# Kernel optimization log

Hardware: AMD Instinct MI355X
Metric: run time of the kernel (lower is better)

## Reference

```python
import jax, jax.numpy as jnp
import numpy as np

S_LOCAL = 3
N_HEADS = 8
EPS = 1e-6


def setup_inputs() -> dict:
    key = jax.random.key(0)
    ks = jax.random.split(key, 9)
    B, D, T, H, W = 2, 512, 96, 16, 16
    std = 0.02
    return {
        "x": jax.random.normal(ks[0], (B, D, T, H, W), dtype=jnp.float32),
        "ln_gamma": jnp.ones((D,), dtype=jnp.float32),
        "ln_beta": jnp.zeros((D,), dtype=jnp.float32),
        "Wq": jax.random.normal(ks[1], (D, D), dtype=jnp.float32) * std,
        "Wk": jax.random.normal(ks[2], (D, D), dtype=jnp.float32) * std,
        "Wv": jax.random.normal(ks[3], (D, D), dtype=jnp.float32) * std,
        "Wkl": jax.random.normal(ks[4], (D, D), dtype=jnp.float32) * std,
        "Wvl": jax.random.normal(ks[5], (D, D), dtype=jnp.float32) * std,
        "Wo": jax.random.normal(ks[6], (D, D), dtype=jnp.float32) * std,
        "q_bias": jax.random.normal(ks[7], (1, N_HEADS, 1, D // N_HEADS), dtype=jnp.float32) * std,
    }


def _unfold_windows(x, s):
    # x: [..., T] -> [..., T, s] sliding windows with zero padding s//2 each side
    p = s // 2
    xp = jnp.pad(x, [(0, 0)] * (x.ndim - 1) + [(p, p)])
    T = x.shape[-1]
    idx = jnp.arange(T)[:, None] + jnp.arange(s)[None, :]  # [T, s]
    return xp[..., idx]


def reference(x, ln_gamma, ln_beta, Wq, Wk, Wv, Wkl, Wvl, Wo, q_bias):
    B, D, T, H, W = x.shape
    nh, dh, s = N_HEADS, D // N_HEADS, S_LOCAL
    factor = dh ** (-0.5)
    N = B * H * W

    # [B,D,T,H,W] -> [N, T, D]
    xt = jnp.transpose(x, (0, 3, 4, 2, 1)).reshape(N, T, D)

    # LayerNorm over D
    mu = xt.mean(-1, keepdims=True)
    var = xt.var(-1, keepdims=True)
    xn = (xt - mu) / jnp.sqrt(var + EPS) * ln_gamma + ln_beta

    # projections -> [N, nh, T, dh]
    def heads(y):
        return jnp.transpose(y.reshape(N, T, nh, dh), (0, 2, 1, 3))

    q = heads(xn @ Wq.T) + q_bias
    k = heads(xn @ Wk.T)
    v = heads(xn @ Wv.T)

    # global attention scores [N, nh, T, T]
    attn_global = jnp.einsum('bhnd,bhgd->bhng', q, k) * factor

    # local k/v: [N, T, D] -> [N, D, T] -> windows [N, D, T, s]
    kl = jnp.transpose(xn @ Wkl.T, (0, 2, 1))
    vl = jnp.transpose(xn @ Wvl.T, (0, 2, 1))
    k_w = jnp.transpose(_unfold_windows(kl, s).reshape(N, nh, dh, T, s), (0, 1, 3, 2, 4))  # [N,nh,T,dh,s]
    v_w = jnp.transpose(_unfold_windows(vl, s).reshape(N, nh, dh, T, s), (0, 1, 3, 2, 4))

    # local mask: True where window element came from zero padding -> [T, s]
    mask_local = _unfold_windows(jnp.ones((T,), dtype=jnp.float32), s) == 0

    attn_local = jnp.einsum('bhnd,bhndl->bhnl', q, k_w)
    attn_local = jnp.where(mask_local, -jnp.inf, attn_local) * factor

    # joint softmax over [T global + s local]
    attn_map = jax.nn.softmax(jnp.concatenate([attn_global, attn_local], axis=-1), axis=-1)
    ag, al = attn_map[..., :T], attn_map[..., T:]

    x_global = jnp.einsum('bhng,bhgd->bhnd', ag, v)
    x_local = jnp.einsum('bhnl,bhndl->bhnd', al, v_w)

    out = (jnp.transpose(x_global + x_local, (0, 2, 1, 3)).reshape(N, T, D)) @ Wo.T
    return jnp.transpose(out.reshape(B, H, W, T, D), (0, 4, 3, 1, 2))
```

## Files before the change

### kernel.cpp

```cpp
#include <hip/hip_runtime.h>
#include <hip/hip_fp16.h>
#include <cstdint>
#include <cstddef>

typedef _Float16 f16;
typedef _Float16 half8 __attribute__((ext_vector_type(8)));
typedef _Float16 half4v __attribute__((ext_vector_type(4)));
typedef float floatx4 __attribute__((ext_vector_type(4)));

#define MTOT 49152

__device__ __forceinline__ void gload_lds16(const f16* g, f16* l) {
  __builtin_amdgcn_global_load_lds((const __attribute__((address_space(1))) void*)g,
                                   (__attribute__((address_space(3))) void*)l, 16, 0, 0);
}

__device__ __forceinline__ half8 load_h8u(const f16* p) {
  half8 v;
  __builtin_memcpy(&v, p, 16);
  return v;
}

__global__ __launch_bounds__(256) void wconv_kernel(
    const float* __restrict__ Wq, const float* __restrict__ Wk,
    const float* __restrict__ Wv, const float* __restrict__ Wkl,
    const float* __restrict__ Wvl, const float* __restrict__ Wo,
    f16* __restrict__ WQKV, f16* __restrict__ WO) {
  int idx = blockIdx.x * 256 + threadIdx.x;
  if (idx < 2560 * 512) {
    int row = idx >> 9;
    int col = idx & 511;
    int seg = row >> 9;
    int r = row & 511;
    const float* src;
    switch (seg) {
      case 0: src = Wq; break;
      case 1: src = Wk; break;
      case 2: src = Wkl; break;
      case 3: src = Wvl; break;
      default: src = Wv; break;
    }
    WQKV[idx] = (f16)src[r * 512 + col];
  }
  if (idx < 512 * 512) WO[idx] = (f16)Wo[idx];
}

__global__ __launch_bounds__(256) void ln_kernel(
    const float* __restrict__ x, const float* __restrict__ gamma,
    const float* __restrict__ beta, f16* __restrict__ XN) {
  const int hwg = blockIdx.x & 3;
  const int t   = (blockIdx.x >> 2) % 96;
  const int b   = blockIdx.x / (4 * 96);
  const int lhw = threadIdx.x & 63;
  const int dg  = threadIdx.x >> 6;
  const int hw  = hwg * 64 + lhw;
  const float* xp = x + (size_t)b * 512 * 24576 + (size_t)t * 256 + hw;

  float s = 0.f, s2 = 0.f;
  for (int d = dg * 128; d < dg * 128 + 128; ++d) {
    float v = xp[(size_t)d * 24576];
    s += v;
    s2 += v * v;
  }
  __shared__ float S1[4][64], S2[4][64];
  S1[dg][lhw] = s;
  S2[dg][lhw] = s2;
  __syncthreads();
  s  = S1[0][lhw] + S1[1][lhw] + S1[2][lhw] + S1[3][lhw];
  s2 = S2[0][lhw] + S2[1][lhw] + S2[2][lhw] + S2[3][lhw];
  const float mean = s * (1.f / 512.f);
  float var = s2 * (1.f / 512.f) - mean * mean;
  var = fmaxf(var, 0.f);
  const float rstd = rsqrtf(var + 1e-6f);
  const int n = b * 256 + hw;
  f16* outp = XN + ((size_t)n * 96 + t) * 512;
  for (int d0 = dg * 128; d0 < dg * 128 + 128; d0 += 8) {
    half8 buf;
#pragma unroll
    for (int j = 0; j < 8; ++j) {
      float v = xp[(size_t)(d0 + j) * 24576];
      buf[j] = (f16)((v - mean) * rstd * gamma[d0 + j] + beta[d0 + j]);
    }
    *(half8*)(outp + d0) = buf;
  }
}

template <int EPI>
__global__ __launch_bounds__(256) void gemm_kernel(
    const f16* __restrict__ A, const f16* __restrict__ B,
    f16* __restrict__ Cqkv, const float* __restrict__ qbias,
    float* __restrict__ Out) {
  __shared__ f16 As[2][128 * 32];
  __shared__ f16 Bs[2][128 * 32];

  const int lin = blockIdx.x;
  const int cpx = (int)gridDim.x >> 3;
  const int o = (lin & 7) * cpx + (lin >> 3);
  int mt, nt;
  if (EPI == 0) {
    mt = o / 20;
    nt = o % 20;
  } else {
    nt = o >> 2;
    mt = o & 3;
  }
  const int m0 = mt * 128;
  const int n0 = nt * 128;
  const int tid = threadIdx.x;
  const int lane = tid & 63;
  const int wid = tid >> 6;
  const int wm = wid >> 1, wn = wid & 1;
  const int l15 = lane & 15, l4 = lane >> 4;

  floatx4 acc[4][4] = {};

  const int srow = tid >> 2;
  const int skp = (((tid & 3) ^ ((tid >> 3) & 3))) * 8;
  const f16* ap = A + (size_t)(m0 + srow) * 512 + skp;
  const f16* bp = B + (size_t)(n0 + srow) * 512 + skp;

  auto stage = [&](int buf, int k0) {
    f16* asl = As[buf] + tid * 8;
    f16* bsl = Bs[buf] + tid * 8;
    gload_lds16(ap + k0, asl);
    gload_lds16(ap + (size_t)64 * 512 + k0, asl + 2048);
    gload_lds16(bp + k0, bsl);
    gload_lds16(bp + (size_t)64 * 512 + k0, bsl + 2048);
  };

  const int rc = (l4 ^ ((l15 >> 1) & 3)) * 8;

  stage(0, 0);
  __syncthreads();
  int cur = 0;
  for (int k0 = 0; k0 < 512; k0 += 32) {
    if (k0 + 32 < 512) stage(cur ^ 1, k0 + 32);
    half8 af[4], bf[4];
#pragma unroll
    for (int mf = 0; mf < 4; ++mf)
      af[mf] = *(const half8*)(As[cur] + (wm * 64 + mf * 16 + l15) * 32 + rc);
#pragma unroll
    for (int nf = 0; nf < 4; ++nf)
      bf[nf] = *(const half8*)(Bs[cur] + (wn * 64 + nf * 16 + l15) * 32 + rc);
#pragma unroll
    for (int mf = 0; mf < 4; ++mf)
#pragma unroll
      for (int nf = 0; nf < 4; ++nf)
        acc[mf][nf] = __builtin_amdgcn_mfma_f32_16x16x32_f16(af[mf], bf[nf], acc[mf][nf], 0, 0, 0);
    __syncthreads();
    cur ^= 1;
  }

  const int mbase = m0 + wm * 64;
  const int nbase = n0 + wn * 64;
  if constexpr (EPI == 0) {
    __shared__ __align__(16) f16 esc[4][16][72];
    float bias[4], scl[4];
#pragma unroll
    for (int nf = 0; nf < 4; ++nf) {
      const int n = nbase + nf * 16 + l15;
      const bool isq = (n < 512);
      bias[nf] = isq ? qbias[n] : 0.0f;
      scl[nf] = isq ? 0.125f : 1.0f;
    }
    const int rrow = lane >> 2;
    const int rcg = lane & 3;
#pragma unroll
    for (int mf = 0; mf < 4; ++mf) {
#pragma unroll
      for (int nf = 0; nf < 4; ++nf)
#pragma unroll
        for (int j = 0; j < 4; ++j)
          esc[wid][l4 * 4 + j][nf * 16 + l15] = (f16)((acc[mf][nf][j] + bias[nf]) * scl[nf]);
      asm volatile("s_waitcnt lgkmcnt(0)" ::: "memory");
      half8 v0 = *(const half8*)(&esc[wid][rrow][rcg * 16]);
      half8 v1 = *(const half8*)(&esc[wid][rrow][rcg * 16 + 8]);
      asm volatile("" ::: "memory");
      f16* dst = Cqkv + (size_t)(mbase + mf * 16 + rrow) * 2560 + nbase + rcg * 16;
      *(half8*)dst = v0;
      *(half8*)(dst + 8) = v1;
    }
  } else {
#pragma unroll
    for (int nf = 0; nf < 4; ++nf) {
      const int m2 = nbase + nf * 16 + l15;
      const int bb = m2 / 24576;
      const int rem = m2 - bb * 24576;
      const int t = rem >> 8;
      const int hw = rem & 255;
      float* op = Out + ((size_t)bb * 512 * 96 + t) * 256 + hw;
#pragma unroll
      for (int mf = 0; mf < 4; ++mf) {
#pragma unroll
        for (int j = 0; j < 4; ++j) {
          const int d = mbase + mf * 16 + l4 * 4 + j;
          __builtin_nontemporal_store(acc[mf][nf][j], op + (size_t)d * 24576);
        }
      }
    }
  }
}

__global__ __launch_bounds__(192) void attn_kernel(
    const f16* __restrict__ QKV, f16* __restrict__ AO, int n0chunk) {
  const int nn = blockIdx.x >> 3;
  const int h = blockIdx.x & 7;
  const int tid = threadIdx.x;
  const int wid = tid >> 6;
  const int lane = tid & 63;
  const int l15 = lane & 15, l4 = lane >> 4;
  const int nglob = n0chunk + nn;
  const int bb = nglob >> 8, hw = nglob & 255;

  __shared__ __align__(16) f16 VTl[64][112];
  __shared__ __align__(16) f16 VLTl[64][112];
  __shared__ __align__(16) float locS[3][16][4];
  __shared__ __align__(16) f16 pS[3][16][104];
  __shared__ __align__(16) f16 pS2[3][16][40];

  const f16* base = QKV + (size_t)nn * 96 * 2560;

#pragma unroll
  for (int it = 0; it < 4; ++it) {
    const int r = (tid >> 3) + it * 24;
    const int c0 = (tid & 7) * 8;
    half8 v  = *(const half8*)(base + (size_t)r * 2560 + 2048 + h * 64 + c0);
    half8 vl = *(const half8*)(base + (size_t)r * 2560 + 1536 + h * 64 + c0);
#pragma unroll
    for (int j = 0; j < 8; ++j) {
      VTl[c0 + j][r]  = v[j];
      VLTl[c0 + j][r] = vl[j];
    }
  }
  if (tid < 128) {
    half8 z = {};
    *(half8*)(&VLTl[tid >> 1][96 + (tid & 1) * 8]) = z;
  }

  half8 kb[6][2];
#pragma unroll
  for (int nf = 0; nf < 6; ++nf)
#pragma unroll
    for (int kg = 0; kg < 2; ++kg)
      kb[nf][kg] = *(const half8*)(base + (size_t)(nf * 16 + l15) * 2560 + 512 + h * 64 + kg * 32 + l4 * 8);

  __syncthreads();

  for (int mb = wid * 2; mb < wid * 2 + 2; ++mb) {
    const int t0 = mb * 16;
    const int tb = (t0 >= 2) ? (t0 - 2) : 0;
    const int d0 = t0 - 1 - tb;

    half8 aq[2], kl1[2], kl2[2];
    {
      int r1 = t0 - 1 + l15; if (r1 < 0) r1 = 0;
      int r2 = t0 + 1 + l15; if (r2 > 95) r2 = 95;
#pragma unroll
      for (int kg = 0; kg < 2; ++kg) {
        aq[kg]  = *(const half8*)(base + (size_t)(t0 + l15) * 2560 + h * 64 + kg * 32 + l4 * 8);
        kl1[kg] = *(const half8*)(base + (size_t)r1 * 2560 + 1024 + h * 64 + kg * 32 + l4 * 8);
        kl2[kg] = *(const half8*)(base + (size_t)r2 * 2560 + 1024 + h * 64 + kg * 32 + l4 * 8);
      }
    }

    floatx4 s[6] = {};
    floatx4 sl1 = {}, sl2 = {};
#pragma unroll
    for (int nf = 0; nf < 6; ++nf)
#pragma unroll
      for (int kg = 0; kg < 2; ++kg)
        s[nf] = __builtin_amdgcn_mfma_f32_16x16x32_f16(aq[kg], kb[nf][kg], s[nf], 0, 0, 0);
#pragma unroll
    for (int kg = 0; kg < 2; ++kg) {
      sl1 = __builtin_amdgcn_mfma_f32_16x16x32_f16(aq[kg], kl1[kg], sl1, 0, 0, 0);
      sl2 = __builtin_amdgcn_mfma_f32_16x16x32_f16(aq[kg], kl2[kg], sl2, 0, 0, 0);
    }

    half8 vb[4][3], vlb[4];
#pragma unroll
    for (int nf = 0; nf < 4; ++nf) {
#pragma unroll
      for (int kg = 0; kg < 3; ++kg)
        vb[nf][kg] = *(const half8*)(&VTl[nf * 16 + l15][kg * 32 + l4 * 8]);
      vlb[nf] = load_h8u(&VLTl[nf * 16 + l15][tb + l4 * 8]);
    }

    {
      half8 z = {};
      f16* pz = &pS2[wid][0][0];
      *(half8*)(pz + lane * 8) = z;
      if (lane < 16) *(half8*)(pz + 512 + lane * 8) = z;
    }
#pragma unroll
    for (int j = 0; j < 4; ++j) {
      const int r = l4 * 4 + j;
      const int s1i = l15 - r;
      if (s1i >= 0 && s1i < 3) locS[wid][r][s1i] = sl1[j];
      const int s2i = l15 + 2 - r;
      if (l15 >= 14 && s2i >= 0 && s2i < 3) locS[wid][r][s2i] = sl2[j];
    }
    __syncthreads();

#pragma unroll
    for (int j = 0; j < 4; ++j) {
      const int row = l4 * 4 + j;
      float sv[6];
#pragma unroll
      for (int nf = 0; nf < 6; ++nf) sv[nf] = s[nf][j];
      float mx = sv[0];
#pragma unroll
      for (int nf = 1; nf < 6; ++nf) mx = fmaxf(mx, sv[nf]);
      for (int off = 1; off < 16; off <<= 1) mx = fmaxf(mx, __shfl_xor(mx, off, 64));
      const float l0 = (t0 + row >= 1)  ? locS[wid][row][0] : -__builtin_inff();
      const float l1 = locS[wid][row][1];
      const float l2 = (t0 + row <= 94) ? locS[wid][row][2] : -__builtin_inff();
      mx = fmaxf(mx, fmaxf(l0, fmaxf(l1, l2)));
      float e[6], sum = 0.f;
#pragma unroll
      for (int nf = 0; nf < 6; ++nf) {
        e[nf] = expf(sv[nf] - mx);
        sum += e[nf];
      }
      for (int off = 1; off < 16; off <<= 1) sum += __shfl_xor(sum, off, 64);
      const float e0 = expf(l0 - mx), e1 = expf(l1 - mx), e2 = expf(l2 - mx);
      sum += e0 + e1 + e2;
      const float rd = 1.0f / sum;
#pragma unroll
      for (int nf = 0; nf < 6; ++nf) pS[wid][row][nf * 16 + l15] = (f16)(e[nf] * rd);
      if (l15 < 3) {
        const int w = row + l15 + d0;
        const float ev = (l15 == 0) ? e0 : ((l15 == 1) ? e1 : e2);
        if (w >= 0) pS2[wid][row][w] = (f16)(ev * rd);
      }
    }
    __syncthreads();

    floatx4 o[4] = {};
    half8 pfr[3];
#pragma unroll
    for (int kg = 0; kg < 3; ++kg)
      pfr[kg] = *(const half8*)(&pS[wid][l15][kg * 32 + l4 * 8]);
    half8 pf2 = *(const half8*)(&pS2[wid][l15][l4 * 8]);
#pragma unroll
    for (int nf = 0; nf < 4; ++nf) {
#pragma unroll
      for (int kg = 0; kg < 3; ++kg)
        o[nf] = __builtin_amdgcn_mfma_f32_16x16x32_f16(pfr[kg], vb[nf][kg], o[nf], 0, 0, 0);
      o[nf] = __builtin_amdgcn_mfma_f32_16x16x32_f16(pf2, vlb[nf], o[nf], 0, 0, 0);
    }

#pragma unroll
    for (int nf = 0; nf < 4; ++nf) {
      const int col = h * 64 + nf * 16 + l15;
#pragma unroll
      for (int j = 0; j < 4; ++j) {
        const int t = t0 + l4 * 4 + j;
        AO[((size_t)(bb * 96 + t) * 256 + hw) * 512 + col] = (f16)o[nf][j];
      }
    }
  }
}

extern "C" void kernel_launch(void* const* d_in, const int* in_sizes, int n_in,
                              void* d_out, int out_size, void* d_ws, size_t ws_size,
                              hipStream_t stream) {
  (void)in_sizes; (void)n_in; (void)out_size;
  const float* x     = (const float*)d_in[0];
  const float* gamma = (const float*)d_in[1];
  const float* beta  = (const float*)d_in[2];
  const float* Wq    = (const float*)d_in[3];
  const float* Wk    = (const float*)d_in[4];
  const float* Wv    = (const float*)d_in[5];
  const float* Wkl   = (const float*)d_in[6];
  const float* Wvl   = (const float*)d_in[7];
  const float* Wo    = (const float*)d_in[8];
  const float* qb    = (const float*)d_in[9];
  float* out = (float*)d_out;

  char* ws = (char*)d_ws;
  size_t off = 0;
  auto alloc = [&](size_t bytes) -> void* {
    void* p = ws + off;
    off += (bytes + 255) & ~(size_t)255;
    return p;
  };
  f16* XN   = (f16*)alloc((size_t)MTOT * 512 * 2);
  f16* AO   = (f16*)alloc((size_t)MTOT * 512 * 2);
  f16* WQKV = (f16*)alloc((size_t)2560 * 512 * 2);
  f16* WOh  = (f16*)alloc((size_t)512 * 512 * 2);
  int cn = 512;
  while (cn > 4 && off + (size_t)cn * 96 * 2560 * 2 + 256 > ws_size)
    cn >>= 1;
  f16* QKVc = (f16*)alloc((size_t)cn * 96 * 2560 * 2);

  wconv_kernel<<<5120, 256, 0, stream>>>(Wq, Wk, Wv, Wkl, Wvl, Wo, WQKV, WOh);
  ln_kernel<<<768, 256, 0, stream>>>(x, gamma, beta, XN);

  const int nch = 512 / cn;
  for (int c = 0; c < nch; ++c) {
    const int ng1 = (cn * 96 / 128) * 20;
    gemm_kernel<0><<<ng1, 256, 0, stream>>>(XN + (size_t)c * cn * 96 * 512, WQKV,
                                            QKVc, qb, nullptr);
    attn_kernel<<<cn * 8, 192, 0, stream>>>(QKVc, AO, c * cn);
  }
  gemm_kernel<1><<<1536, 256, 0, stream>>>(WOh, AO, nullptr, nullptr, out);
}
```

Measured before the change: 439.2 us.

## Replace QKV projection GEMM with 256x256-tile, 8-wave, ping-pong pipelined kernel

Splits the templated GEMM into a dedicated QKV-projection kernel and an output-projection kernel. The QKV kernel uses 256x256 tiles with K-step 64, 512 threads, direct global-to-LDS loads staged in quarter-tiles between MFMA phases, and s_setprio to interleave memory and compute. Larger tiles raise arithmetic intensity and cut redundant A/B fetches. The cost is much higher LDS and register pressure and tighter chunk-size constraints, with the minimum chunk raised to 32.

Result: faster. 423.7 us (-3.5%).

```diff
diff --git a/kernel.cpp b/kernel.cpp
--- a/kernel.cpp
+++ b/kernel.cpp
@@ -85,10 +85,173 @@
   }
 }
 
-template <int EPI>
-__global__ __launch_bounds__(256) void gemm_kernel(
+__global__ __launch_bounds__(512, 2) void gemmA_kernel(
     const f16* __restrict__ A, const f16* __restrict__ B,
-    f16* __restrict__ Cqkv, const float* __restrict__ qbias,
+    f16* __restrict__ Cqkv, const float* __restrict__ qbias) {
+  __shared__ f16 LA[2][256 * 64];
+  __shared__ f16 LB[2][256 * 64];
+  __shared__ __align__(16) f16 esc[8][16][72];
+
+  const int lin = blockIdx.x;
+  const int cpx = (int)gridDim.x >> 3;
+  const int swz = (lin & 7) * cpx + (lin >> 3);
+  const int o = ((gridDim.x & 7) == 0) ? swz : lin;
+  const int mt = o / 10;
+  const int nt = o % 10;
+  const int m0 = mt * 256;
+  const int n0 = nt * 256;
+
+  const int tid = threadIdx.x;
+  const int wid = tid >> 6;
+  const int lane = tid & 63;
+  const int wm = wid >> 2;
+  const int wn = wid & 3;
+  const int l15 = lane & 15, l4 = lane >> 4;
+
+  const int srow = tid >> 3;
+  const int scol = ((tid & 7) ^ (srow & 7)) * 8;
+  const f16* Abase = A + (size_t)(m0 + srow) * 512 + scol;
+  const f16* Bbase = B + (size_t)(n0 + srow) * 512 + scol;
+
+  const int cks0 = ((l4) ^ (l15 & 7)) * 8;
+  const int cks1 = ((4 + l4) ^ (l15 & 7)) * 8;
+  const int arow = wm * 128 + l15;
+  const int brow = wn * 64 + l15;
+
+  floatx4 acc[8][4] = {};
+  half8 a_f[4][2];
+  half8 b_f[4][2];
+
+  auto stageH = [&](int slot, int kt, int mat, int h) {
+    const f16* g = (mat ? Bbase : Abase) + kt * 64 + (size_t)(h * 128) * 512;
+    f16* l = (mat ? LB[slot] : LA[slot]) + h * 8192 + tid * 8;
+    gload_lds16(g, l);
+    gload_lds16(g + (size_t)64 * 512, l + 4096);
+  };
+
+  stageH(0, 0, 0, 0); stageH(0, 0, 0, 1);
+  stageH(0, 0, 1, 0); stageH(0, 0, 1, 1);
+  stageH(1, 1, 0, 0);
+  asm volatile("s_waitcnt vmcnt(2)" ::: "memory");
+  __builtin_amdgcn_s_barrier();
+
+#pragma unroll
+  for (int kt = 0; kt < 8; ++kt) {
+    const f16* As = LA[kt & 1];
+    const f16* Bs = LB[kt & 1];
+    const int nsl = (kt + 1) & 1;
+
+#pragma unroll
+    for (int mf2 = 0; mf2 < 4; ++mf2) {
+      a_f[mf2][0] = *(const half8*)(As + (arow + mf2 * 16) * 64 + cks0);
+      a_f[mf2][1] = *(const half8*)(As + (arow + mf2 * 16) * 64 + cks1);
+    }
+#pragma unroll
+    for (int nf = 0; nf < 2; ++nf) {
+      b_f[nf][0] = *(const half8*)(Bs + (brow + nf * 16) * 64 + cks0);
+      b_f[nf][1] = *(const half8*)(Bs + (brow + nf * 16) * 64 + cks1);
+    }
+    if (kt + 1 < 8) stageH(nsl, kt + 1, 0, 1);
+    __builtin_amdgcn_s_barrier();
+    __builtin_amdgcn_s_setprio(1);
+#pragma unroll
+    for (int mf2 = 0; mf2 < 4; ++mf2)
+#pragma unroll
+      for (int nf2 = 0; nf2 < 2; ++nf2)
+#pragma unroll
+        for (int ks = 0; ks < 2; ++ks)
+          acc[mf2][nf2] = __builtin_amdgcn_mfma_f32_16x16x32_f16(
+              a_f[mf2][ks], b_f[nf2][ks], acc[mf2][nf2], 0, 0, 0);
+    __builtin_amdgcn_s_setprio(0);
+    __builtin_amdgcn_s_barrier();
+
+#pragma unroll
+    for (int nf = 2; nf < 4; ++nf) {
+      b_f[nf][0] = *(const half8*)(Bs + (brow + nf * 16) * 64 + cks0);
+      b_f[nf][1] = *(const half8*)(Bs + (brow + nf * 16) * 64 + cks1);
+    }
+    if (kt + 1 < 8) stageH(nsl, kt + 1, 1, 0);
+    __builtin_amdgcn_s_barrier();
+    __builtin_amdgcn_s_setprio(1);
+#pragma unroll
+    for (int mf2 = 0; mf2 < 4; ++mf2)
+#pragma unroll
+      for (int nf2 = 0; nf2 < 2; ++nf2)
+#pragma unroll
+        for (int ks = 0; ks < 2; ++ks)
+          acc[mf2][2 + nf2] = __builtin_amdgcn_mfma_f32_16x16x32_f16(
+              a_f[mf2][ks], b_f[2 + nf2][ks], acc[mf2][2 + nf2], 0, 0, 0);
+    __builtin_amdgcn_s_setprio(0);
+    __builtin_amdgcn_s_barrier();
+
+#pragma unroll
+    for (int mf2 = 0; mf2 < 4; ++mf2) {
+      a_f[mf2][0] = *(const half8*)(As + (arow + 64 + mf2 * 16) * 64 + cks0);
+      a_f[mf2][1] = *(const half8*)(As + (arow + 64 + mf2 * 16) * 64 + cks1);
+    }
+    if (kt + 1 < 8) stageH(nsl, kt + 1, 1, 1);
+    __builtin_amdgcn_s_barrier();
+    __builtin_amdgcn_s_setprio(1);
+#pragma unroll
+    for (int mf2 = 0; mf2 < 4; ++mf2)
+#pragma unroll
+      for (int nf2 = 0; nf2 < 2; ++nf2)
+#pragma unroll
+        for (int ks = 0; ks < 2; ++ks)
+          acc[4 + mf2][nf2] = __builtin_amdgcn_mfma_f32_16x16x32_f16(
+              a_f[mf2][ks], b_f[nf2][ks], acc[4 + mf2][nf2], 0, 0, 0);
+    __builtin_amdgcn_s_setprio(0);
+    __builtin_amdgcn_s_barrier();
+
+    if (kt + 2 < 8) stageH(kt & 1, kt + 2, 0, 0);
+    __builtin_amdgcn_s_barrier();
+    __builtin_amdgcn_s_setprio(1);
+#pragma unroll
+    for (int mf2 = 0; mf2 < 4; ++mf2)
+#pragma unroll
+      for (int nf2 = 0; nf2 < 2; ++nf2)
+#pragma unroll
+        for (int ks = 0; ks < 2; ++ks)
+          acc[4 + mf2][2 + nf2] = __builtin_amdgcn_mfma_f32_16x16x32_f16(
+              a_f[mf2][ks], b_f[2 + nf2][ks], acc[4 + mf2][2 + nf2], 0, 0, 0);
+    __builtin_amdgcn_s_setprio(0);
+    if (kt < 6) {
+      asm volatile("s_waitcnt vmcnt(2)" ::: "memory");
+    } else if (kt == 6) {
+      asm volatile("s_waitcnt vmcnt(0)" ::: "memory");
+    }
+    __builtin_amdgcn_s_barrier();
+  }
+
+  float bias[4], scl[4];
+#pragma unroll
+  for (int nf = 0; nf < 4; ++nf) {
+    const int n = n0 + wn * 64 + nf * 16 + l15;
+    const bool isq = (n < 512);
+    bias[nf] = isq ? qbias[n] : 0.0f;
+    scl[nf]  = isq ? 0.125f : 1.0f;
+  }
+  const int rrow = lane >> 2;
+  const int rcg  = lane & 3;
+#pragma unroll
+  for (int mf = 0; mf < 8; ++mf) {
+#pragma unroll
+    for (int nf = 0; nf < 4; ++nf)
+#pragma unroll
+      for (int j = 0; j < 4; ++j)
+        esc[wid][l4 * 4 + j][nf * 16 + l15] = (f16)((acc[mf][nf][j] + bias[nf]) * scl[nf]);
+    asm volatile("s_waitcnt lgkmcnt(0)" ::: "memory");
+    half8 v0 = *(const half8*)(&esc[wid][rrow][rcg * 16]);
+    half8 v1 = *(const half8*)(&esc[wid][rrow][rcg * 16 + 8]);
+    asm volatile("" ::: "memory");
+    f16* dst = Cqkv + (size_t)(m0 + wm * 128 + mf * 16 + rrow) * 2560 + n0 + wn * 64 + rcg * 16;
+    *(half8*)dst = v0;
+    *(half8*)(dst + 8) = v1;
+  }
+}
+
+__global__ __launch_bounds__(256) void gemmO_kernel(
+    const f16* __restrict__ A, const f16* __restrict__ B,
     float* __restrict__ Out) {
   __shared__ f16 As[2][128 * 32];
   __shared__ f16 Bs[2][128 * 32];
@@ -96,14 +259,8 @@
   const int lin = blockIdx.x;
   const int cpx = (int)gridDim.x >> 3;
   const int o = (lin & 7) * cpx + (lin >> 3);
-  int mt, nt;
-  if (EPI == 0) {
-    mt = o / 20;
-    nt = o % 20;
-  } else {
-    nt = o >> 2;
-    mt = o & 3;
-  }
+  const int nt = o >> 2;
+  const int mt = o & 3;
   const int m0 = mt * 128;
   const int n0 = nt * 128;
   const int tid = threadIdx.x;
@@ -153,49 +310,20 @@
 
   const int mbase = m0 + wm * 64;
   const int nbase = n0 + wn * 64;
-  if constexpr (EPI == 0) {
-    __shared__ __align__(16) f16 esc[4][16][72];
-    float bias[4], scl[4];
-#pragma unroll
-    for (int nf = 0; nf < 4; ++nf) {
-      const int n = nbase + nf * 16 + l15;
-      const bool isq = (n < 512);
-      bias[nf] = isq ? qbias[n] : 0.0f;
-      scl[nf] = isq ? 0.125f : 1.0f;
-    }
-    const int rrow = lane >> 2;
-    const int rcg = lane & 3;
+#pragma unroll
+  for (int nf = 0; nf < 4; ++nf) {
+    const int m2 = nbase + nf * 16 + l15;
+    const int bb = m2 / 24576;
+    const int rem = m2 - bb * 24576;
+    const int t = rem >> 8;
+    const int hw = rem & 255;
+    float* op = Out + ((size_t)bb * 512 * 96 + t) * 256 + hw;
 #pragma unroll
     for (int mf = 0; mf < 4; ++mf) {
 #pragma unroll
-      for (int nf = 0; nf < 4; ++nf)
-#pragma unroll
-        for (int j = 0; j < 4; ++j)
-          esc[wid][l4 * 4 + j][nf * 16 + l15] = (f16)((acc[mf][nf][j] + bias[nf]) * scl[nf]);
-      asm volatile("s_waitcnt lgkmcnt(0)" ::: "memory");
-      half8 v0 = *(const half8*)(&esc[wid][rrow][rcg * 16]);
-      half8 v1 = *(const half8*)(&esc[wid][rrow][rcg * 16 + 8]);
-      asm volatile("" ::: "memory");
-      f16* dst = Cqkv + (size_t)(mbase + mf * 16 + rrow) * 2560 + nbase + rcg * 16;
-      *(half8*)dst = v0;
-      *(half8*)(dst + 8) = v1;
-    }
-  } else {
-#pragma unroll
-    for (int nf = 0; nf < 4; ++nf) {
-      const int m2 = nbase + nf * 16 + l15;
-      const int bb = m2 / 24576;
-      const int rem = m2 - bb * 24576;
-      const int t = rem >> 8;
-      const int hw = rem & 255;
-      float* op = Out + ((size_t)bb * 512 * 96 + t) * 256 + hw;
-#pragma unroll
-      for (int mf = 0; mf < 4; ++mf) {
-#pragma unroll
-        for (int j = 0; j < 4; ++j) {
-          const int d = mbase + mf * 16 + l4 * 4 + j;
-          __builtin_nontemporal_store(acc[mf][nf][j], op + (size_t)d * 24576);
-        }
+      for (int j = 0; j < 4; ++j) {
+        const int d = mbase + mf * 16 + l4 * 4 + j;
+        __builtin_nontemporal_store(acc[mf][nf][j], op + (size_t)d * 24576);
       }
     }
   }
@@ -389,7 +517,7 @@
   f16* WQKV = (f16*)alloc((size_t)2560 * 512 * 2);
   f16* WOh  = (f16*)alloc((size_t)512 * 512 * 2);
   int cn = 512;
-  while (cn > 4 && off + (size_t)cn * 96 * 2560 * 2 + 256 > ws_size)
+  while (cn > 32 && off + (size_t)cn * 96 * 2560 * 2 + 256 > ws_size)
     cn >>= 1;
   f16* QKVc = (f16*)alloc((size_t)cn * 96 * 2560 * 2);
 
@@ -398,10 +526,10 @@
 
   const int nch = 512 / cn;
   for (int c = 0; c < nch; ++c) {
-    const int ng1 = (cn * 96 / 128) * 20;
-    gemm_kernel<0><<<ng1, 256, 0, stream>>>(XN + (size_t)c * cn * 96 * 512, WQKV,
-                                            QKVc, qb, nullptr);
+    const int mtiles = (cn * 96) / 256;
+    gemmA_kernel<<<mtiles * 10, 512, 0, stream>>>(XN + (size_t)c * cn * 96 * 512,
+                                                  WQKV, QKVc, qb);
     attn_kernel<<<cn * 8, 192, 0, stream>>>(QKVc, AO, c * cn);
   }
-  gemm_kernel<1><<<1536, 256, 0, stream>>>(WOh, AO, nullptr, nullptr, out);
-}
+  gemmO_kernel<<<1536, 256, 0, stream>>>(WOh, AO, out);
+}
```
